# Kernel tuning notes

Hardware: AMD Instinct MI355X
Metric: run time of the kernel (lower is better)

## Reference

```python
import jax, jax.numpy as jnp
import numpy as np

V = 196608   # HEALPix nside=128 pixels
NNZ = 9 * V  # ~8 neighbors + self loop per pixel
B, FIN, FOUT, K = 4, 32, 64, 5


def setup_inputs() -> dict:
    key = jax.random.key(0)
    k1, k2, k3, k4, k5, k6 = jax.random.split(key, 6)
    lap_rows = jax.random.randint(k1, (NNZ,), 0, V, dtype=jnp.int32)
    lap_cols = jax.random.randint(k2, (NNZ,), 0, V, dtype=jnp.int32)
    # scale values so the Chebyshev recurrence stays numerically tame
    lap_vals = jax.random.normal(k3, (NNZ,), dtype=jnp.float32) * 0.1
    inputs = jax.random.normal(k4, (B, V, FIN), dtype=jnp.float32)
    std = np.sqrt(2.0 / (FIN + FOUT)).astype(np.float32)  # xavier normal
    weight = jax.random.normal(k5, (K, FIN, FOUT), dtype=jnp.float32) * std
    bias = jnp.full((FOUT,), 0.01, dtype=jnp.float32)
    return {"lap_rows": lap_rows, "lap_cols": lap_cols, "lap_vals": lap_vals,
            "inputs": inputs, "weight": weight, "bias": bias}


def reference(lap_rows, lap_cols, lap_vals, inputs, weight, bias):
    Bq, Vq, Fin = inputs.shape
    Kq, _, Fout = weight.shape

    # x0: [V, Fin*B]  (matches torch permute(1,2,0).reshape)
    x0 = jnp.transpose(inputs, (1, 2, 0)).reshape(Vq, Fin * Bq)

    def spmm(x):  # sparse [V,V] @ dense [V, Fin*B] via gather + scatter-add
        contrib = lap_vals[:, None] * x[lap_cols]  # [nnz, Fin*B]
        return jax.ops.segment_sum(contrib, lap_rows, num_segments=Vq)

    xs = [x0]
    if Kq > 1:
        xs.append(spmm(x0))
    for _ in range(2, Kq):
        xs.append(2.0 * spmm(xs[-1]) - xs[-2])
    cheb = jnp.stack(xs)  # [K, V, Fin*B]

    # [K,V,Fin,B] -> [B,V,Fin,K] -> [B*V, Fin*K]
    cheb = cheb.reshape(Kq, Vq, Fin, Bq).transpose(3, 1, 2, 0).reshape(Bq * Vq, Fin * Kq)
    # torch weight.view(Fin*K, Fout) flattens (K,Fin) row-major -> reshape(K*Fin, Fout)
    w2 = weight.reshape(Kq * Fin, Fout)
    out = (cheb @ w2).reshape(Bq, Vq, Fout)
    return out + bias
```

## Files before the change

kernel.cpp:

```cpp
#include <hip/hip_runtime.h>

#define V 196608
#define NNZ (9 * V)
#define B 4
#define FIN 32
#define FOUT 64
#define K 5
#define C 128
#define ROWU 64
#define SPMM_BLOCKS 2048

typedef __attribute__((ext_vector_type(8))) short bf16x8;
typedef __attribute__((ext_vector_type(4))) float f32x4;

static __device__ __forceinline__ unsigned int f2bf(float f) {
    union { float f; unsigned int u; } v; v.f = f;
    return (v.u + 0x7FFFu + ((v.u >> 16) & 1u)) >> 16;
}
static __device__ __forceinline__ float bflo(unsigned int u) {
    union { unsigned int u; float f; } v; v.u = u << 16; return v.f;
}
static __device__ __forceinline__ float bfhi(unsigned int u) {
    union { unsigned int u; float f; } v; v.u = u & 0xFFFF0000u; return v.f;
}

__global__ void zero_cursor(uint4* __restrict__ p) {
    int t = blockIdx.x * 256 + threadIdx.x;
    if (t < V / 4) p[t] = (uint4){0u, 0u, 0u, 0u};
}

__global__ void build_x0(const float* __restrict__ inp, uint4* __restrict__ x0v) {
    int t = blockIdx.x * 256 + threadIdx.x;
    if (t >= V * 16) return;
    int v = t >> 4;
    int seg = t & 15;
    int b = seg >> 2;
    int q = seg & 3;
    const float4* s = reinterpret_cast<const float4*>(inp + ((size_t)b * V + v) * 32 + q * 8);
    float4 fa = s[0], fb = s[1];
    uint4 u;
    u.x = f2bf(fa.x) | (f2bf(fa.y) << 16);
    u.y = f2bf(fa.z) | (f2bf(fa.w) << 16);
    u.z = f2bf(fb.x) | (f2bf(fb.y) << 16);
    u.w = f2bf(fb.z) | (f2bf(fb.w) << 16);
    x0v[(size_t)v * 16 + seg] = u;
}

__global__ void build_wfrag(const float* __restrict__ w, uint4* __restrict__ wfh,
                            uint4* __restrict__ wfl) {
    int idx = blockIdx.x * 256 + threadIdx.x;
    if (idx >= K * 4 * 64) return;
    int lane = idx & 63;
    int nt = (idx >> 6) & 3;
    int k = idx >> 8;
    int col = lane & 15;
    int quad = lane >> 4;
    int o = nt * 16 + col;
    unsigned int hh[8], ll[8];
#pragma unroll
    for (int e = 0; e < 8; ++e) {
        int fin = quad * 8 + e;
        float wv = w[(fin * 5 + k) * 64 + o];
        unsigned int hb = f2bf(wv);
        float hf = bflo(hb);
        ll[e] = f2bf(wv - hf);
        hh[e] = hb;
    }
    uint4 uh, ul;
    uh.x = hh[0] | (hh[1] << 16);
    uh.y = hh[2] | (hh[3] << 16);
    uh.z = hh[4] | (hh[5] << 16);
    uh.w = hh[6] | (hh[7] << 16);
    ul.x = ll[0] | (ll[1] << 16);
    ul.y = ll[2] | (ll[3] << 16);
    ul.z = ll[4] | (ll[5] << 16);
    ul.w = ll[6] | (ll[7] << 16);
    wfh[idx] = uh;
    wfl[idx] = ul;
}

__global__ void hist_rows(const int* __restrict__ rows, int* __restrict__ cnt) {
    int e = blockIdx.x * 256 + threadIdx.x;
    if (e < NNZ) atomicAdd(&cnt[rows[e]], 1);
}

__global__ void chunk_sums(const int* __restrict__ cnt, int* __restrict__ bsum) {
    __shared__ int ws[16];
    int tid = threadIdx.x;
    int lane = tid & 63;
    int wid = tid >> 6;
    int v = cnt[blockIdx.x * 1024 + tid];
#pragma unroll
    for (int off = 32; off >= 1; off >>= 1) v += __shfl_down(v, off, 64);
    if (lane == 0) ws[wid] = v;
    __syncthreads();
    if (tid < 16) {
        int s = ws[tid];
#pragma unroll
        for (int off = 8; off >= 1; off >>= 1) s += __shfl_down(s, off, 16);
        if (tid == 0) bsum[blockIdx.x] = s;
    }
}

__global__ void scan_sums(const int* __restrict__ bsum, int* __restrict__ bpre,
                          int* __restrict__ rowptr) {
    __shared__ int ws[4];
    int tid = threadIdx.x;
    int lane = tid & 63;
    int wid = tid >> 6;
    int v = (tid < 192) ? bsum[tid] : 0;
    int x = v;
#pragma unroll
    for (int off = 1; off < 64; off <<= 1) {
        int t = __shfl_up(x, off, 64);
        if (lane >= off) x += t;
    }
    if (lane == 63) ws[wid] = x;
    __syncthreads();
    if (wid == 0 && lane < 4) {
        int s = ws[lane];
        int y = s;
#pragma unroll
        for (int off = 1; off < 4; off <<= 1) {
            int t = __shfl_up(y, off, 4);
            if (lane >= off) y += t;
        }
        ws[lane] = y - s;
    }
    __syncthreads();
    int incl = x + ws[wid];
    if (tid < 192) bpre[tid] = incl - v;
    if (tid == 191) rowptr[V] = incl;
}

__global__ void scan_chunks(const int* __restrict__ cnt, const int* __restrict__ bpre,
                            int* __restrict__ rowptr, int* __restrict__ cursor) {
    __shared__ int wsum[16];
    int tid = threadIdx.x;
    int lane = tid & 63;
    int wid = tid >> 6;
    int base = blockIdx.x * 1024;
    int v = cnt[base + tid];
    int x = v;
#pragma unroll
    for (int off = 1; off < 64; off <<= 1) {
        int t = __shfl_up(x, off, 64);
        if (lane >= off) x += t;
    }
    if (lane == 63) wsum[wid] = x;
    __syncthreads();
    if (wid == 0 && lane < 16) {
        int s = wsum[lane];
        int y = s;
#pragma unroll
        for (int off = 1; off < 16; off <<= 1) {
            int t = __shfl_up(y, off, 16);
            if (lane >= off) y += t;
        }
        wsum[lane] = y - s;
    }
    __syncthreads();
    int excl = x - v + wsum[wid] + bpre[blockIdx.x];
    rowptr[base + tid] = excl;
    cursor[base + tid] = excl;
}

__global__ void scatter_edges_win(const int* __restrict__ rows, const int* __restrict__ cols,
                                  const float* __restrict__ vals, int* __restrict__ cursor,
                                  int2* __restrict__ cev, int lo, int hi) {
    int e = blockIdx.x * 256 + threadIdx.x;
    if (e >= NNZ) return;
    int r = rows[e];
    if (r < lo || r >= hi) return;
    int p = atomicAdd(&cursor[r], 1);
    int2 pk;
    pk.x = cols[e];
    pk.y = __float_as_int(vals[e]);
    cev[p] = pk;
}

template <int COMBINE>
__global__ __launch_bounds__(256) void spmm_gather(
    const int* __restrict__ rowptr, const int2* __restrict__ cev,
    const unsigned int* __restrict__ x, const unsigned int* __restrict__ xm2,
    unsigned int* __restrict__ y) {
    const int lane = threadIdx.x & 63;
    const int wid0 = (blockIdx.x * 256 + threadIdx.x) >> 6;
    const int NW = SPMM_BLOCKS * 4;
    for (int base = wid0 * 2; base < V; base += NW * 2) {
        const int r0 = base, r1 = base + 1;
        const int s0 = rowptr[r0];
        const int e0 = rowptr[r0 + 1];
        const int e1 = rowptr[r1 + 1];
        float ax0 = 0.f, ay0 = 0.f, ax1 = 0.f, ay1 = 0.f;
        int i0 = s0, i1 = e0;
        while (e0 - i0 >= 4 && e1 - i1 >= 4) {
            int2 Ea[4], Eb[4];
#pragma unroll
            for (int j = 0; j < 4; ++j) {
                Ea[j] = cev[i0 + j];
                Eb[j] = cev[i1 + j];
            }
            unsigned int Ua[4], Ub[4];
#pragma unroll
            for (int j = 0; j < 4; ++j) {
                Ua[j] = x[(size_t)Ea[j].x * ROWU + lane];
                Ub[j] = x[(size_t)Eb[j].x * ROWU + lane];
            }
#pragma unroll
            for (int j = 0; j < 4; ++j) {
                float va = __int_as_float(Ea[j].y);
                float vb = __int_as_float(Eb[j].y);
                ax0 = fmaf(va, bflo(Ua[j]), ax0);
                ay0 = fmaf(va, bfhi(Ua[j]), ay0);
                ax1 = fmaf(vb, bflo(Ub[j]), ax1);
                ay1 = fmaf(vb, bfhi(Ub[j]), ay1);
            }
            i0 += 4;
            i1 += 4;
        }
        while (e0 - i0 >= 4) {
            int2 Ea[4];
#pragma unroll
            for (int j = 0; j < 4; ++j) Ea[j] = cev[i0 + j];
            unsigned int Ua[4];
#pragma unroll
            for (int j = 0; j < 4; ++j) Ua[j] = x[(size_t)Ea[j].x * ROWU + lane];
#pragma unroll
            for (int j = 0; j < 4; ++j) {
                float va = __int_as_float(Ea[j].y);
                ax0 = fmaf(va, bflo(Ua[j]), ax0);
                ay0 = fmaf(va, bfhi(Ua[j]), ay0);
            }
            i0 += 4;
        }
        while (e1 - i1 >= 4) {
            int2 Eb[4];
#pragma unroll
            for (int j = 0; j < 4; ++j) Eb[j] = cev[i1 + j];
            unsigned int Ub[4];
#pragma unroll
            for (int j = 0; j < 4; ++j) Ub[j] = x[(size_t)Eb[j].x * ROWU + lane];
#pragma unroll
            for (int j = 0; j < 4; ++j) {
                float vb = __int_as_float(Eb[j].y);
                ax1 = fmaf(vb, bflo(Ub[j]), ax1);
                ay1 = fmaf(vb, bfhi(Ub[j]), ay1);
            }
            i1 += 4;
        }
        for (; i0 + 2 <= e0; i0 += 2) {
            int2 a = cev[i0], b = cev[i0 + 1];
            unsigned int u0 = x[(size_t)a.x * ROWU + lane];
            unsigned int u1 = x[(size_t)b.x * ROWU + lane];
            float v0 = __int_as_float(a.y), v1 = __int_as_float(b.y);
            ax0 = fmaf(v0, bflo(u0), ax0);
            ay0 = fmaf(v0, bfhi(u0), ay0);
            ax0 = fmaf(v1, bflo(u1), ax0);
            ay0 = fmaf(v1, bfhi(u1), ay0);
        }
        for (; i0 < e0; ++i0) {
            int2 a = cev[i0];
            unsigned int u = x[(size_t)a.x * ROWU + lane];
            float v = __int_as_float(a.y);
            ax0 = fmaf(v, bflo(u), ax0);
            ay0 = fmaf(v, bfhi(u), ay0);
        }
        for (; i1 + 2 <= e1; i1 += 2) {
            int2 a = cev[i1], b = cev[i1 + 1];
            unsigned int u0 = x[(size_t)a.x * ROWU + lane];
            unsigned int u1 = x[(size_t)b.x * ROWU + lane];
            float v0 = __int_as_float(a.y), v1 = __int_as_float(b.y);
            ax1 = fmaf(v0, bflo(u0), ax1);
            ay1 = fmaf(v0, bfhi(u0), ay1);
            ax1 = fmaf(v1, bflo(u1), ax1);
            ay1 = fmaf(v1, bfhi(u1), ay1);
        }
        for (; i1 < e1; ++i1) {
            int2 a = cev[i1];
            unsigned int u = x[(size_t)a.x * ROWU + lane];
            float v = __int_as_float(a.y);
            ax1 = fmaf(v, bflo(u), ax1);
            ay1 = fmaf(v, bfhi(u), ay1);
        }
        if (COMBINE) {
            unsigned int m0 = xm2[(size_t)r0 * ROWU + lane];
            unsigned int m1 = xm2[(size_t)r1 * ROWU + lane];
            ax0 = 2.0f * ax0 - bflo(m0);
            ay0 = 2.0f * ay0 - bfhi(m0);
            ax1 = 2.0f * ax1 - bflo(m1);
            ay1 = 2.0f * ay1 - bfhi(m1);
        }
        y[(size_t)r0 * ROWU + lane] = f2bf(ax0) | (f2bf(ay0) << 16);
        y[(size_t)r1 * ROWU + lane] = f2bf(ax1) | (f2bf(ay1) << 16);
    }
}

__global__ __launch_bounds__(256) void fused_mfma(
    const unsigned short* __restrict__ x0, const unsigned short* __restrict__ x1,
    const unsigned short* __restrict__ x2, const unsigned short* __restrict__ x3,
    const unsigned short* __restrict__ x4, const uint4* __restrict__ wfh,
    const uint4* __restrict__ wfl, const float* __restrict__ bias,
    float* __restrict__ out) {
    const int tid = threadIdx.x;
    const int lane = tid & 63;
    const int g = (blockIdx.x * 256 + tid) >> 6;
    const int v0 = g << 4;
    const int col = lane & 15;
    const int quad = lane >> 4;
    const unsigned short* const xs[K] = {x0, x1, x2, x3, x4};

    f32x4 acc[B][4];
#pragma unroll
    for (int b = 0; b < B; ++b)
#pragma unroll
        for (int nt = 0; nt < 4; ++nt) acc[b][nt] = (f32x4){0.f, 0.f, 0.f, 0.f};

#pragma unroll
    for (int k = 0; k < K; ++k) {
        const unsigned short* xk = xs[k] + ((size_t)(v0 + col)) * C + quad * 8;
        bf16x8 a0 = *reinterpret_cast<const bf16x8*>(xk);
        bf16x8 a1 = *reinterpret_cast<const bf16x8*>(xk + 32);
        bf16x8 a2 = *reinterpret_cast<const bf16x8*>(xk + 64);
        bf16x8 a3 = *reinterpret_cast<const bf16x8*>(xk + 96);
#pragma unroll
        for (int nt = 0; nt < 4; ++nt) {
            uint4 uh = wfh[(k * 4 + nt) * 64 + lane];
            uint4 ul = wfl[(k * 4 + nt) * 64 + lane];
            bf16x8 wh = *reinterpret_cast<bf16x8*>(&uh);
            bf16x8 wl = *reinterpret_cast<bf16x8*>(&ul);
            acc[0][nt] = __builtin_amdgcn_mfma_f32_16x16x32_bf16(a0, wh, acc[0][nt], 0, 0, 0);
            acc[1][nt] = __builtin_amdgcn_mfma_f32_16x16x32_bf16(a1, wh, acc[1][nt], 0, 0, 0);
            acc[2][nt] = __builtin_amdgcn_mfma_f32_16x16x32_bf16(a2, wh, acc[2][nt], 0, 0, 0);
            acc[3][nt] = __builtin_amdgcn_mfma_f32_16x16x32_bf16(a3, wh, acc[3][nt], 0, 0, 0);
            acc[0][nt] = __builtin_amdgcn_mfma_f32_16x16x32_bf16(a0, wl, acc[0][nt], 0, 0, 0);
            acc[1][nt] = __builtin_amdgcn_mfma_f32_16x16x32_bf16(a1, wl, acc[1][nt], 0, 0, 0);
            acc[2][nt] = __builtin_amdgcn_mfma_f32_16x16x32_bf16(a2, wl, acc[2][nt], 0, 0, 0);
            acc[3][nt] = __builtin_amdgcn_mfma_f32_16x16x32_bf16(a3, wl, acc[3][nt], 0, 0, 0);
        }
    }

    float bv[4];
#pragma unroll
    for (int nt = 0; nt < 4; ++nt) bv[nt] = bias[nt * 16 + col];
#pragma unroll
    for (int b = 0; b < B; ++b)
#pragma unroll
        for (int nt = 0; nt < 4; ++nt)
#pragma unroll
            for (int r = 0; r < 4; ++r) {
                int row = quad * 4 + r;
                out[((size_t)b * V + v0 + row) * FOUT + nt * 16 + col] = acc[b][nt][r] + bv[nt];
            }
}

extern "C" void kernel_launch(void* const* d_in, const int* in_sizes, int n_in,
                              void* d_out, int out_size, void* d_ws, size_t ws_size,
                              hipStream_t stream) {
    const int* lap_rows = (const int*)d_in[0];
    const int* lap_cols = (const int*)d_in[1];
    const float* lap_vals = (const float*)d_in[2];
    const float* inputs = (const float*)d_in[3];
    const float* weight = (const float*)d_in[4];
    const float* bias = (const float*)d_in[5];
    float* out = (float*)d_out;

    char* p = (char*)d_ws;
    auto alloc = [&](size_t bytes) {
        char* r = p;
        p += (bytes + 511) & ~(size_t)511;
        return r;
    };
    int* rowptr = (int*)alloc((size_t)(V + 1) * 4);
    int* cursor = (int*)alloc((size_t)V * 4);
    int* bsum = (int*)alloc(192 * 4);
    int* bpre = (int*)alloc(192 * 4);
    uint4* wfh = (uint4*)alloc((size_t)K * 4 * 64 * 16);
    uint4* wfl = (uint4*)alloc((size_t)K * 4 * 64 * 16);
    int2* cev = (int2*)alloc((size_t)NNZ * 8);
    unsigned int* xb0 = (unsigned int*)alloc((size_t)V * ROWU * 4);
    unsigned int* xb1 = (unsigned int*)alloc((size_t)V * ROWU * 4);
    unsigned int* xb2 = (unsigned int*)alloc((size_t)V * ROWU * 4);
    unsigned int* xb3 = (unsigned int*)alloc((size_t)V * ROWU * 4);
    unsigned int* xb4 = (unsigned int*)alloc((size_t)V * ROWU * 4);

    const int edge_blocks = (NNZ + 255) / 256;
    const int x0_blocks = (V * 16 + 255) / 256;
    const int mfma_blocks = (V / 16) * 64 / 256;

    zero_cursor<<<(V / 4 + 255) / 256, 256, 0, stream>>>((uint4*)cursor);
    hist_rows<<<edge_blocks, 256, 0, stream>>>(lap_rows, cursor);
    chunk_sums<<<V / 1024, 1024, 0, stream>>>(cursor, bsum);
    scan_sums<<<1, 256, 0, stream>>>(bsum, bpre, rowptr);
    scan_chunks<<<V / 1024, 1024, 0, stream>>>(cursor, bpre, rowptr, cursor);
    for (int w = 0; w < 4; ++w) {
        scatter_edges_win<<<edge_blocks, 256, 0, stream>>>(
            lap_rows, lap_cols, lap_vals, cursor, cev, w * (V / 4), (w + 1) * (V / 4));
    }

    build_x0<<<x0_blocks, 256, 0, stream>>>(inputs, (uint4*)xb0);
    build_wfrag<<<5, 256, 0, stream>>>(weight, wfh, wfl);

    spmm_gather<0><<<SPMM_BLOCKS, 256, 0, stream>>>(rowptr, cev, xb0, nullptr, xb1);
    spmm_gather<1><<<SPMM_BLOCKS, 256, 0, stream>>>(rowptr, cev, xb1, xb0, xb2);
    spmm_gather<1><<<SPMM_BLOCKS, 256, 0, stream>>>(rowptr, cev, xb2, xb1, xb3);
    spmm_gather<1><<<SPMM_BLOCKS, 256, 0, stream>>>(rowptr, cev, xb3, xb2, xb4);

    fused_mfma<<<mfma_blocks, 256, 0, stream>>>(
        (const unsigned short*)xb0, (const unsigned short*)xb1, (const unsigned short*)xb2,
        (const unsigned short*)xb3, (const unsigned short*)xb4, wfh, wfl, bias, out);
}
```

Baseline: 630.2 us.

## Record per-edge rank in histogram to replace atomic scatter with rank-based placement

The histogram kernel now saves each edge's atomicAdd return value as its rank within its row. The CSR scatter then computes each edge's position as rowptr plus rank without any atomics, which removes the four windowed atomic scatter passes. One fused launch of 8 output windows times 864 edge slices replaces them, and each window filters writes to its own region of the output. In exchange the change adds an NNZ-sized rank buffer that costs an extra write and read, and each edge is reread eight times across the windows.

```diff
diff --git a/kernel.cpp b/kernel.cpp
--- a/kernel.cpp
+++ b/kernel.cpp
@@ -9,6 +9,8 @@
 #define C 128
 #define ROWU 64
 #define SPMM_BLOCKS 2048
+#define NSLICE 864
+#define EDGES_PER_SLICE 2048
 
 typedef __attribute__((ext_vector_type(8))) short bf16x8;
 typedef __attribute__((ext_vector_type(4))) float f32x4;
@@ -79,9 +81,10 @@
     wfl[idx] = ul;
 }
 
-__global__ void hist_rows(const int* __restrict__ rows, int* __restrict__ cnt) {
+__global__ void hist_rank(const int* __restrict__ rows, int* __restrict__ cnt,
+                          int* __restrict__ rank) {
     int e = blockIdx.x * 256 + threadIdx.x;
-    if (e < NNZ) atomicAdd(&cnt[rows[e]], 1);
+    if (e < NNZ) rank[e] = atomicAdd(&cnt[rows[e]], 1);
 }
 
 __global__ void chunk_sums(const int* __restrict__ cnt, int* __restrict__ bsum) {
@@ -134,7 +137,7 @@
 }
 
 __global__ void scan_chunks(const int* __restrict__ cnt, const int* __restrict__ bpre,
-                            int* __restrict__ rowptr, int* __restrict__ cursor) {
+                            int* __restrict__ rowptr) {
     __shared__ int wsum[16];
     int tid = threadIdx.x;
     int lane = tid & 63;
@@ -162,21 +165,27 @@
     __syncthreads();
     int excl = x - v + wsum[wid] + bpre[blockIdx.x];
     rowptr[base + tid] = excl;
-    cursor[base + tid] = excl;
-}
-
-__global__ void scatter_edges_win(const int* __restrict__ rows, const int* __restrict__ cols,
-                                  const float* __restrict__ vals, int* __restrict__ cursor,
-                                  int2* __restrict__ cev, int lo, int hi) {
-    int e = blockIdx.x * 256 + threadIdx.x;
-    if (e >= NNZ) return;
-    int r = rows[e];
-    if (r < lo || r >= hi) return;
-    int p = atomicAdd(&cursor[r], 1);
-    int2 pk;
-    pk.x = cols[e];
-    pk.y = __float_as_int(vals[e]);
-    cev[p] = pk;
+}
+
+__global__ void scatter_rank(const int* __restrict__ rows, const int* __restrict__ cols,
+                             const float* __restrict__ vals, const int* __restrict__ rowptr,
+                             const int* __restrict__ rank, int2* __restrict__ cev) {
+    const int slice = blockIdx.x >> 3;
+    const int w = blockIdx.x & 7;
+    const int lo = w * (NNZ / 8);
+    const int hi = lo + (NNZ / 8);
+    const int base = slice * EDGES_PER_SLICE;
+#pragma unroll 2
+    for (int i = threadIdx.x; i < EDGES_PER_SLICE; i += 256) {
+        int e = base + i;
+        int p = rowptr[rows[e]] + rank[e];
+        if (p >= lo && p < hi) {
+            int2 pk;
+            pk.x = cols[e];
+            pk.y = __float_as_int(vals[e]);
+            cev[p] = pk;
+        }
+    }
 }
 
 template <int COMBINE>
@@ -372,9 +381,10 @@
         return r;
     };
     int* rowptr = (int*)alloc((size_t)(V + 1) * 4);
-    int* cursor = (int*)alloc((size_t)V * 4);
+    int* cnt = (int*)alloc((size_t)V * 4);
     int* bsum = (int*)alloc(192 * 4);
     int* bpre = (int*)alloc(192 * 4);
+    int* rank = (int*)alloc((size_t)NNZ * 4);
     uint4* wfh = (uint4*)alloc((size_t)K * 4 * 64 * 16);
     uint4* wfl = (uint4*)alloc((size_t)K * 4 * 64 * 16);
     int2* cev = (int2*)alloc((size_t)NNZ * 8);
@@ -388,15 +398,13 @@
     const int x0_blocks = (V * 16 + 255) / 256;
     const int mfma_blocks = (V / 16) * 64 / 256;
 
-    zero_cursor<<<(V / 4 + 255) / 256, 256, 0, stream>>>((uint4*)cursor);
-    hist_rows<<<edge_blocks, 256, 0, stream>>>(lap_rows, cursor);
-    chunk_sums<<<V / 1024, 1024, 0, stream>>>(cursor, bsum);
+    zero_cursor<<<(V / 4 + 255) / 256, 256, 0, stream>>>((uint4*)cnt);
+    hist_rank<<<edge_blocks, 256, 0, stream>>>(lap_rows, cnt, rank);
+    chunk_sums<<<V / 1024, 1024, 0, stream>>>(cnt, bsum);
     scan_sums<<<1, 256, 0, stream>>>(bsum, bpre, rowptr);
-    scan_chunks<<<V / 1024, 1024, 0, stream>>>(cursor, bpre, rowptr, cursor);
-    for (int w = 0; w < 4; ++w) {
-        scatter_edges_win<<<edge_blocks, 256, 0, stream>>>(
-            lap_rows, lap_cols, lap_vals, cursor, cev, w * (V / 4), (w + 1) * (V / 4));
-    }
+    scan_chunks<<<V / 1024, 1024, 0, stream>>>(cnt, bpre, rowptr);
+    scatter_rank<<<NSLICE * 8, 256, 0, stream>>>(lap_rows, lap_cols, lap_vals, rowptr,
+                                                 rank, cev);
 
     build_x0<<<x0_blocks, 256, 0, stream>>>(inputs, (uint4*)xb0);
     build_wfrag<<<5, 256, 0, stream>>>(weight, wfh, wfl);
```

Result: no change. 628.7 us (-0.2%).
